# Kernel optimization log

Measured on AMD Instinct MI355X. Metric: run time of the kernel, lower is better.

Reference implementation:

```python
import jax, jax.numpy as jnp
import numpy as np

D_MODEL = 1024
NHEAD = 16
HEAD_DIM = D_MODEL // NHEAD
D_FF = 4096
EPS = 1e-5


def _layernorm(x, g, b):
    mu = jnp.mean(x, axis=-1, keepdims=True)
    var = jnp.mean((x - mu) ** 2, axis=-1, keepdims=True)
    return (x - mu) * jax.lax.rsqrt(var + EPS) * g + b


def setup_inputs() -> dict:
    key = jax.random.key(0)
    ks = jax.random.split(key, 13)
    s = 1.0 / np.sqrt(D_MODEL)
    sf = 1.0 / np.sqrt(D_FF)
    # weights stored as [in, out] (transposed torch Linear)
    return {
        "src": jax.random.normal(ks[0], (4, 2048, D_MODEL), jnp.float32),
        "Wq": jax.random.uniform(ks[1], (D_MODEL, D_MODEL), jnp.float32, -s, s),
        "bq": jnp.zeros((D_MODEL,), jnp.float32),
        "Wk": jax.random.uniform(ks[2], (D_MODEL, D_MODEL), jnp.float32, -s, s),
        "bk": jnp.zeros((D_MODEL,), jnp.float32),
        "Wv": jax.random.uniform(ks[3], (D_MODEL, D_MODEL), jnp.float32, -s, s),
        "bv": jnp.zeros((D_MODEL,), jnp.float32),
        "Wo": jax.random.uniform(ks[4], (D_MODEL, D_MODEL), jnp.float32, -s, s),
        "bo": jnp.zeros((D_MODEL,), jnp.float32),
        "W1": jax.random.uniform(ks[5], (D_MODEL, D_FF), jnp.float32, -s, s),
        "b1": jnp.zeros((D_FF,), jnp.float32),
        "W2": jax.random.uniform(ks[6], (D_FF, D_MODEL), jnp.float32, -sf, sf),
        "b2": jnp.zeros((D_MODEL,), jnp.float32),
        "g1": jnp.ones((D_MODEL,), jnp.float32),
        "be1": jnp.zeros((D_MODEL,), jnp.float32),
        "g2": jnp.ones((D_MODEL,), jnp.float32),
        "be2": jnp.zeros((D_MODEL,), jnp.float32),
    }


def reference(src, Wq, bq, Wk, bk, Wv, bv, Wo, bo, W1, b1, W2, b2, g1, be1, g2, be2):
    B, S, _ = src.shape
    scale = 1.0 / np.sqrt(HEAD_DIM)
    # project and split heads: [B, H, S, Dh]
    def heads(W, b):
        return (src @ W + b).reshape(B, S, NHEAD, HEAD_DIM).transpose(0, 2, 1, 3)
    Q, K, V = heads(Wq, bq), heads(Wk, bk), heads(Wv, bv)
    scores = jnp.einsum('bhqd,bhkd->bhqk', Q, K) * scale
    attn = jax.nn.softmax(scores, axis=-1)
    ctx = jnp.einsum('bhqk,bhkd->bhqd', attn, V)
    ctx = ctx.transpose(0, 2, 1, 3).reshape(B, S, D_MODEL)
    attn_out = ctx @ Wo + bo
    x = _layernorm(src + attn_out, g1, be1)
    ff = jax.nn.relu(x @ W1 + b1) @ W2 + b2
    return _layernorm(x + ff, g2, be2)
```

## Files before the change

### kernel.cpp

```cpp
#include <hip/hip_runtime.h>

typedef __attribute__((ext_vector_type(8))) short bf16x8;
typedef __attribute__((ext_vector_type(4))) float f32x4;
typedef unsigned short u16;
typedef unsigned int u32;

__device__ __forceinline__ u16 f2b(float f) {
  u32 u = __float_as_uint(f);
  u = (u + 0x7fffu + ((u >> 16) & 1u)) >> 16;
  return (u16)u;
}
__device__ __forceinline__ float b2f(u16 b) {
  return __uint_as_float(((u32)b) << 16);
}
__device__ __forceinline__ u32 cvtpk_bf16(float lo, float hi) {
  u32 r;
  asm("v_cvt_pk_bf16_f32 %0, %1, %2" : "=v"(r) : "v"(lo), "v"(hi));
  return r;
}
__device__ __forceinline__ void gload_lds16(const u16* g, u16* l) {
  __builtin_amdgcn_global_load_lds(
      (const __attribute__((address_space(1))) void*)g,
      (__attribute__((address_space(3))) void*)l, 16, 0, 0);
}

__device__ __forceinline__ void tr_tile(const float* __restrict__ in,
                                        u16* __restrict__ out, int R, int C,
                                        int bx, int by, int tid) {
  __shared__ float t[32][33];
  int tx = tid & 31, ty = tid >> 5;
  int rb = by * 32, cb = bx * 32;
  for (int i = 0; i < 4; i++)
    t[ty + i * 8][tx] = in[(size_t)(rb + ty + i * 8) * C + cb + tx];
  __syncthreads();
  for (int i = 0; i < 4; i++)
    out[(size_t)(cb + ty + i * 8) * R + rb + tx] = f2b(t[tx][ty + i * 8]);
}

__global__ __launch_bounds__(256) void prep(
    const float* __restrict__ src, u16* __restrict__ XB,
    const float* __restrict__ Wq, const float* __restrict__ Wk,
    const float* __restrict__ Wv, const float* __restrict__ Wo,
    const float* __restrict__ W1, const float* __restrict__ W2,
    u16* __restrict__ WQKVT, u16* __restrict__ WOT, u16* __restrict__ W1T,
    u16* __restrict__ W2T, const float* __restrict__ bq,
    const float* __restrict__ bk, const float* __restrict__ bv,
    float* __restrict__ bqkv) {
  const int blk = blockIdx.x, tid = threadIdx.x;
  if (blk < 8192) {
    int i = blk * 256 + tid;
    float4 v = ((const float4*)src)[i];
    ushort4 o;
    o.x = f2b(v.x); o.y = f2b(v.y); o.z = f2b(v.z); o.w = f2b(v.w);
    ((ushort4*)XB)[i] = o;
  } else if (blk < 8192 + 4096) {
    int t = blk - 8192;
    int w = t >> 10, tt = t & 1023;
    const float* in = (w == 0) ? Wq : (w == 1) ? Wk : (w == 2) ? Wv : Wo;
    u16* out = (w == 3) ? WOT : (WQKVT + (size_t)w * 1024 * 1024);
    tr_tile(in, out, 1024, 1024, tt & 31, tt >> 5, tid);
  } else if (blk < 8192 + 4096 + 4096) {
    int t = blk - (8192 + 4096);
    tr_tile(W1, W1T, 1024, 4096, t & 127, t >> 7, tid);
  } else if (blk < 8192 + 4096 + 4096 + 4096) {
    int t = blk - (8192 + 4096 + 4096);
    tr_tile(W2, W2T, 4096, 1024, t & 31, t >> 5, tid);
  } else {
    int i = (blk - (8192 + 4096 + 4096 + 4096)) * 256 + tid;
    if (i < 3072)
      bqkv[i] = i < 1024 ? bq[i] : (i < 2048 ? bk[i - 1024] : bv[i - 2048]);
  }
}

__device__ __forceinline__ void stage_quarter(const u16* __restrict__ src,
                                              size_t rowbase, int K, int kcol,
                                              u16* dst, int c, int srow, int sg,
                                              int wid) {
  int row_ = c * 64 + srow;
  int gs_ = sg ^ (row_ & 7);
  gload_lds16(src + (rowbase + row_) * K + kcol + gs_ * 8,
              &dst[(c * 64 + wid * 8) * 64]);
}

template <bool PF>
__device__ __forceinline__ void tile_step(
    const u16* sAc, const u16* sBc, u16* sAn, u16* sBn,
    const u16* __restrict__ A, const u16* __restrict__ Bt, size_t abase,
    size_t bbase, int K, int Tn, int wm, int wn, int l16, int lq, int srow,
    int sg, int wid, f32x4 (&acc)[8][4]) {
  __syncthreads();
#pragma unroll
  for (int ks = 0; ks < 2; ++ks) {
    bf16x8 Bf[4], Af[4];
#pragma unroll
    for (int j = 0; j < 4; ++j) {
      int r = wn * 64 + j * 16 + l16;
      Bf[j] = *(const bf16x8*)&sBc[r * 64 + (((ks * 4 + lq) ^ (r & 7)) << 3)];
    }
#pragma unroll
    for (int i = 0; i < 4; ++i) {
      int r = wm * 128 + i * 16 + l16;
      Af[i] = *(const bf16x8*)&sAc[r * 64 + (((ks * 4 + lq) ^ (r & 7)) << 3)];
    }
    if (PF) {
      const u16* src = (ks == 0) ? A : Bt;
      size_t rb = (ks == 0) ? abase : bbase;
      u16* dst = (ks == 0) ? sAn : sBn;
      stage_quarter(src, rb, K, Tn * 64, dst, 0, srow, sg, wid);
      stage_quarter(src, rb, K, Tn * 64, dst, 1, srow, sg, wid);
    }
    __builtin_amdgcn_s_setprio(1);
#pragma unroll
    for (int i = 0; i < 4; ++i)
#pragma unroll
      for (int j = 0; j < 4; ++j)
        acc[i][j] = __builtin_amdgcn_mfma_f32_16x16x32_bf16(Af[i], Bf[j],
                                                            acc[i][j], 0, 0, 0);
    __builtin_amdgcn_s_setprio(0);
#pragma unroll
    for (int i = 0; i < 4; ++i) {
      int r = wm * 128 + 64 + i * 16 + l16;
      Af[i] = *(const bf16x8*)&sAc[r * 64 + (((ks * 4 + lq) ^ (r & 7)) << 3)];
    }
    if (PF) {
      const u16* src = (ks == 0) ? A : Bt;
      size_t rb = (ks == 0) ? abase : bbase;
      u16* dst = (ks == 0) ? sAn : sBn;
      stage_quarter(src, rb, K, Tn * 64, dst, 2, srow, sg, wid);
      stage_quarter(src, rb, K, Tn * 64, dst, 3, srow, sg, wid);
    }
    __builtin_amdgcn_s_setprio(1);
#pragma unroll
    for (int i = 0; i < 4; ++i)
#pragma unroll
      for (int j = 0; j < 4; ++j)
        acc[4 + i][j] = __builtin_amdgcn_mfma_f32_16x16x32_bf16(
            Af[i], Bf[j], acc[4 + i][j], 0, 0, 0);
    __builtin_amdgcn_s_setprio(0);
  }
}

template <int MODE>
__global__ __launch_bounds__(512, 1) void gemm256(const u16* __restrict__ A,
                                                  const u16* __restrict__ Bt,
                                                  const float* __restrict__ bias,
                                                  void* __restrict__ out,
                                                  int M, int N, int K,
                                                  float oscale) {
  __shared__ u16 sA0[256 * 64];
  __shared__ u16 sB0[256 * 64];
  __shared__ u16 sA1[256 * 64];
  __shared__ u16 sB1[256 * 64];
  const int tid = threadIdx.x, lane = tid & 63, wid = tid >> 6;
  const int l16 = lane & 15, lq = lane >> 4;
  const int wm = wid >> 2, wn = wid & 3;
  const size_t abase = (size_t)blockIdx.x * 256;
  const size_t bbase = (size_t)blockIdx.y * 256;
  const int srow = tid >> 3;
  const int sg = tid & 7;
  const int nt = K >> 6;

  f32x4 acc[8][4];
#pragma unroll
  for (int i = 0; i < 8; ++i)
#pragma unroll
    for (int j = 0; j < 4; ++j) acc[i][j] = (f32x4){0.f, 0.f, 0.f, 0.f};

#pragma unroll
  for (int c = 0; c < 4; ++c) {
    stage_quarter(A, abase, K, 0, sA0, c, srow, sg, wid);
    stage_quarter(Bt, bbase, K, 0, sB0, c, srow, sg, wid);
  }

  int T = 0;
  for (; T + 2 < nt; T += 2) {
    tile_step<true>(sA0, sB0, sA1, sB1, A, Bt, abase, bbase, K, T + 1, wm, wn,
                    l16, lq, srow, sg, wid, acc);
    tile_step<true>(sA1, sB1, sA0, sB0, A, Bt, abase, bbase, K, T + 2, wm, wn,
                    l16, lq, srow, sg, wid, acc);
  }
  tile_step<true>(sA0, sB0, sA1, sB1, A, Bt, abase, bbase, K, nt - 1, wm, wn,
                  l16, lq, srow, sg, wid, acc);
  tile_step<false>(sA1, sB1, sA0, sB0, A, Bt, abase, bbase, K, 0, wm, wn, l16,
                   lq, srow, sg, wid, acc);

  const int gmb = blockIdx.x * 256 + wm * 128;
  const int gnb = blockIdx.y * 256 + wn * 64;
#pragma unroll
  for (int i = 0; i < 8; ++i) {
    int gm0 = gmb + i * 16 + lq * 4;
#pragma unroll
    for (int j = 0; j < 4; ++j) {
      int gn = gnb + j * 16 + l16;
      float bv = bias[gn];
#pragma unroll
      for (int r = 0; r < 4; ++r) {
        float v = acc[i][j][r] + bv;
        ((u16*)out)[(size_t)(gm0 + r) * N + gn] = f2b(v > 0.f ? v : 0.f);
      }
    }
  }
}

template <bool PF>
__device__ __forceinline__ void tile_stepR(
    const u16* sAc, const u16* sBc, u16* sAn, u16* sBn,
    const u16* __restrict__ A, const u16* __restrict__ Bt, size_t abase,
    size_t bbase, int K, int Tn, int wm, int wn, int l16, int lq, int srow,
    int sg, int wid, f32x4 (&acc)[4][4]) {
  __syncthreads();
#pragma unroll
  for (int ks = 0; ks < 2; ++ks) {
    bf16x8 Bf[4], Af[4];
#pragma unroll
    for (int j = 0; j < 4; ++j) {
      int r = wn * 64 + j * 16 + l16;
      Bf[j] = *(const bf16x8*)&sBc[r * 64 + (((ks * 4 + lq) ^ (r & 7)) << 3)];
    }
#pragma unroll
    for (int i = 0; i < 4; ++i) {
      int r = wm * 64 + i * 16 + l16;
      Af[i] = *(const bf16x8*)&sAc[r * 64 + (((ks * 4 + lq) ^ (r & 7)) << 3)];
    }
    if (PF) {
      if (ks == 0) {
        stage_quarter(A, abase, K, Tn * 64, sAn, 0, srow, sg, wid);
        stage_quarter(A, abase, K, Tn * 64, sAn, 1, srow, sg, wid);
        stage_quarter(Bt, bbase, K, Tn * 64, sBn, 0, srow, sg, wid);
      } else {
        stage_quarter(Bt, bbase, K, Tn * 64, sBn, 1, srow, sg, wid);
        stage_quarter(Bt, bbase, K, Tn * 64, sBn, 2, srow, sg, wid);
        stage_quarter(Bt, bbase, K, Tn * 64, sBn, 3, srow, sg, wid);
      }
    }
    __builtin_amdgcn_s_setprio(1);
#pragma unroll
    for (int i = 0; i < 4; ++i)
#pragma unroll
      for (int j = 0; j < 4; ++j)
        acc[i][j] = __builtin_amdgcn_mfma_f32_16x16x32_bf16(Af[i], Bf[j],
                                                            acc[i][j], 0, 0, 0);
    __builtin_amdgcn_s_setprio(0);
  }
}

template <int MODE>
__global__ __launch_bounds__(512, 1) void gemmR(const u16* __restrict__ A,
                                                const u16* __restrict__ Bt,
                                                const float* __restrict__ bias,
                                                void* __restrict__ out,
                                                int M, int N, int K,
                                                float oscale) {
  __shared__ u16 sA0[128 * 64];
  __shared__ u16 sB0[256 * 64];
  __shared__ u16 sA1[128 * 64];
  __shared__ u16 sB1[256 * 64];
  const int tid = threadIdx.x, lane = tid & 63, wid = tid >> 6;
  const int l16 = lane & 15, lq = lane >> 4;
  const int wm = wid >> 2, wn = wid & 3;
  const size_t abase = (size_t)blockIdx.x * 128;
  const size_t bbase = (size_t)blockIdx.y * 256;
  const int srow = tid >> 3;
  const int sg = tid & 7;
  const int nt = K >> 6;

  f32x4 acc[4][4];
#pragma unroll
  for (int i = 0; i < 4; ++i)
#pragma unroll
    for (int j = 0; j < 4; ++j) acc[i][j] = (f32x4){0.f, 0.f, 0.f, 0.f};

#pragma unroll
  for (int c = 0; c < 2; ++c) stage_quarter(A, abase, K, 0, sA0, c, srow, sg, wid);
#pragma unroll
  for (int c = 0; c < 4; ++c) stage_quarter(Bt, bbase, K, 0, sB0, c, srow, sg, wid);

  int T = 0;
  for (; T + 2 < nt; T += 2) {
    tile_stepR<true>(sA0, sB0, sA1, sB1, A, Bt, abase, bbase, K, T + 1, wm, wn,
                     l16, lq, srow, sg, wid, acc);
    tile_stepR<true>(sA1, sB1, sA0, sB0, A, Bt, abase, bbase, K, T + 2, wm, wn,
                     l16, lq, srow, sg, wid, acc);
  }
  tile_stepR<true>(sA0, sB0, sA1, sB1, A, Bt, abase, bbase, K, nt - 1, wm, wn,
                   l16, lq, srow, sg, wid, acc);
  tile_stepR<false>(sA1, sB1, sA0, sB0, A, Bt, abase, bbase, K, 0, wm, wn, l16,
                    lq, srow, sg, wid, acc);

  const int gmb = blockIdx.x * 128 + wm * 64;
  const int gnb = blockIdx.y * 256 + wn * 64;
#pragma unroll
  for (int i = 0; i < 4; ++i) {
    int gm0 = gmb + i * 16 + lq * 4;
#pragma unroll
    for (int j = 0; j < 4; ++j) {
      int gn = gnb + j * 16 + l16;
      float bv = bias[gn];
      if constexpr (MODE == 1) {
#pragma unroll
        for (int r = 0; r < 4; ++r)
          ((u16*)out)[(size_t)(gm0 + r) * N + gn] = f2b(acc[i][j][r] + bv);
      } else {
        int sel = gn >> 10;
        int h = (gn & 1023) >> 6, d = gn & 63;
        int b = gm0 >> 11, s = gm0 & 2047;
        u16* o = (u16*)out + (size_t)sel * (8u << 20);
        if (sel == 2) {
          ushort4 w;
          w.x = f2b(acc[i][j][0] + bv);
          w.y = f2b(acc[i][j][1] + bv);
          w.z = f2b(acc[i][j][2] + bv);
          w.w = f2b(acc[i][j][3] + bv);
          *(ushort4*)(o + ((size_t)((b * 16 + h) * 64 + d)) * 2048 + s) = w;
        } else {
          float sc = (sel == 0) ? oscale : 1.f;
#pragma unroll
          for (int r = 0; r < 4; ++r)
            o[((size_t)(b * 16 + h) * 2048 + s + r) * 64 + d] =
                f2b((acc[i][j][r] + bv) * sc);
        }
      }
    }
  }
}

__global__ __launch_bounds__(512) void attn_fwd(const u16* __restrict__ Q,
                                                const u16* __restrict__ Kb,
                                                const u16* __restrict__ Vt,
                                                u16* __restrict__ ctx) {
  __shared__ u16 sK[64][64];
  __shared__ u16 sV[64][64];
  __shared__ u16 sP[8][16][72];
  const int tid = threadIdx.x, lane = tid & 63, wid = tid >> 6;
  const int l16 = lane & 15, lq = lane >> 4;
  const int bh = blockIdx.y, qt = blockIdx.x;
  const size_t base = (size_t)bh * (2048 * 64);
  const int xk = l16 & 7;

  bf16x8 qf[2];
  {
    int qrow = qt * 128 + wid * 16 + l16;
    qf[0] = *(const bf16x8*)(Q + base + (size_t)qrow * 64 + lq * 8);
    qf[1] = *(const bf16x8*)(Q + base + (size_t)qrow * 64 + 32 + lq * 8);
  }
  f32x4 o[4];
#pragma unroll
  for (int j = 0; j < 4; j++) o[j] = (f32x4){0.f, 0.f, 0.f, 0.f};
  float lrow = 0.f;

  const int srow = tid >> 3;
  const int sg8 = ((tid & 7) ^ (srow & 7)) * 8;
  const int wslot = (tid & 7) * 8;

  const u16* kp = Kb + base + (size_t)srow * 64 + sg8;
  const u16* vp = Vt + base + (size_t)srow * 2048 + sg8;

  uint4 rk = *(const uint4*)kp;
  uint4 rv = *(const uint4*)vp;

  for (int kv0 = 0; kv0 < 2048; kv0 += 64) {
    __syncthreads();
    *(uint4*)&sK[srow][wslot] = rk;
    *(uint4*)&sV[srow][wslot] = rv;
    if (kv0 + 64 < 2048) {
      int kn = kv0 + 64;
      rk = *(const uint4*)(kp + (size_t)kn * 64);
      rv = *(const uint4*)(vp + kn);
    }
    __syncthreads();

    f32x4 sf[4];
#pragma unroll
    for (int j = 0; j < 4; j++) sf[j] = (f32x4){0.f, 0.f, 0.f, 0.f};
    __builtin_amdgcn_s_setprio(1);
#pragma unroll
    for (int ks = 0; ks < 2; ks++)
#pragma unroll
      for (int j = 0; j < 4; j++) {
        bf16x8 kf = *(const bf16x8*)&sK[j * 16 + l16][((ks * 4 + lq) ^ xk) * 8];
        sf[j] = __builtin_amdgcn_mfma_f32_16x16x32_bf16(kf, qf[ks], sf[j], 0, 0, 0);
      }
    __builtin_amdgcn_s_setprio(0);

#pragma unroll
    for (int j = 0; j < 4; j++) {
      float p0 = __builtin_amdgcn_exp2f(sf[j][0]);
      float p1 = __builtin_amdgcn_exp2f(sf[j][1]);
      float p2 = __builtin_amdgcn_exp2f(sf[j][2]);
      float p3 = __builtin_amdgcn_exp2f(sf[j][3]);
      lrow += (p0 + p1) + (p2 + p3);
      uint2 w;
      w.x = cvtpk_bf16(p0, p1);
      w.y = cvtpk_bf16(p2, p3);
      *(uint2*)&sP[wid][l16][j * 16 + lq * 4] = w;
    }

    __builtin_amdgcn_s_setprio(1);
#pragma unroll
    for (int ks = 0; ks < 2; ks++) {
      bf16x8 pf = *(const bf16x8*)&sP[wid][l16][ks * 32 + lq * 8];
#pragma unroll
      for (int j = 0; j < 4; j++) {
        bf16x8 vf = *(const bf16x8*)&sV[j * 16 + l16][((ks * 4 + lq) ^ xk) * 8];
        o[j] = __builtin_amdgcn_mfma_f32_16x16x32_bf16(pf, vf, o[j], 0, 0, 0);
      }
    }
    __builtin_amdgcn_s_setprio(0);
  }

  lrow += __shfl_xor(lrow, 16);
  lrow += __shfl_xor(lrow, 32);
  float lval[4];
#pragma unroll
  for (int r = 0; r < 4; r++) lval[r] = 1.f / __shfl(lrow, lq * 4 + r);
  const int b = bh >> 4, h = bh & 15;
#pragma unroll
  for (int j = 0; j < 4; j++)
#pragma unroll
    for (int r = 0; r < 4; r++) {
      int srw = qt * 128 + wid * 16 + lq * 4 + r;
      int d = j * 16 + l16;
      ctx[((size_t)(b * 2048 + srw)) * 1024 + h * 64 + d] = f2b(o[j][r] * lval[r]);
    }
}

template <int A_BF16, int B_BF16, int WRITE_F32>
__global__ __launch_bounds__(256) void ln_res(const void* __restrict__ a,
                                              const void* __restrict__ bsrc,
                                              const float* __restrict__ g,
                                              const float* __restrict__ be,
                                              float* __restrict__ outf,
                                              u16* __restrict__ outb) {
  const int row = blockIdx.x, tid = threadIdx.x;
  const size_t off = (size_t)row * 1024 + tid * 4;
  float4 x;
  if constexpr (A_BF16) {
    ushort4 av = *(const ushort4*)((const u16*)a + off);
    x.x = b2f(av.x); x.y = b2f(av.y); x.z = b2f(av.z); x.w = b2f(av.w);
  } else {
    x = *(const float4*)((const float*)a + off);
  }
  if constexpr (B_BF16) {
    ushort4 bv = *(const ushort4*)((const u16*)bsrc + off);
    x.x += b2f(bv.x); x.y += b2f(bv.y); x.z += b2f(bv.z); x.w += b2f(bv.w);
  } else {
    float4 bb = *(const float4*)((const float*)bsrc + off);
    x.x += bb.x; x.y += bb.y; x.z += bb.z; x.w += bb.w;
  }
  float s = x.x + x.y + x.z + x.w;
  float s2 = x.x * x.x + x.y * x.y + x.z * x.z + x.w * x.w;
  for (int o = 1; o < 64; o <<= 1) {
    s += __shfl_xor(s, o);
    s2 += __shfl_xor(s2, o);
  }
  __shared__ float rbuf[8];
  int lane = tid & 63, wid = tid >> 6;
  if (lane == 0) { rbuf[wid] = s; rbuf[4 + wid] = s2; }
  __syncthreads();
  s = rbuf[0] + rbuf[1] + rbuf[2] + rbuf[3];
  s2 = rbuf[4] + rbuf[5] + rbuf[6] + rbuf[7];
  float mu = s * (1.f / 1024.f);
  float var = s2 * (1.f / 1024.f) - mu * mu;
  float rstd = rsqrtf(var + 1e-5f);
  int c = tid * 4;
  float y0 = (x.x - mu) * rstd * g[c + 0] + be[c + 0];
  float y1 = (x.y - mu) * rstd * g[c + 1] + be[c + 1];
  float y2 = (x.z - mu) * rstd * g[c + 2] + be[c + 2];
  float y3 = (x.w - mu) * rstd * g[c + 3] + be[c + 3];
  if constexpr (WRITE_F32) {
    float4 y; y.x = y0; y.y = y1; y.z = y2; y.w = y3;
    *(float4*)(outf + off) = y;
  } else {
    ushort4 yb;
    yb.x = f2b(y0); yb.y = f2b(y1); yb.z = f2b(y2); yb.w = f2b(y3);
    *(ushort4*)(outb + off) = yb;
  }
}

extern "C" void kernel_launch(void* const* d_in, const int* in_sizes, int n_in,
                              void* d_out, int out_size, void* d_ws, size_t ws_size,
                              hipStream_t stream) {
  const float* src = (const float*)d_in[0];
  const float* Wq = (const float*)d_in[1];
  const float* bq = (const float*)d_in[2];
  const float* Wk = (const float*)d_in[3];
  const float* bk = (const float*)d_in[4];
  const float* Wv = (const float*)d_in[5];
  const float* bv = (const float*)d_in[6];
  const float* Wo = (const float*)d_in[7];
  const float* bo = (const float*)d_in[8];
  const float* W1 = (const float*)d_in[9];
  const float* b1 = (const float*)d_in[10];
  const float* W2 = (const float*)d_in[11];
  const float* b2 = (const float*)d_in[12];
  const float* g1 = (const float*)d_in[13];
  const float* be1 = (const float*)d_in[14];
  const float* g2 = (const float*)d_in[15];
  const float* be2 = (const float*)d_in[16];
  float* out = (float*)d_out;
  char* ws = (char*)d_ws;
  const size_t MB = 1ull << 20;

  u16* XB    = (u16*)(ws + 0);
  u16* WQKVT = (u16*)(ws + 16 * MB);
  u16* WOT   = (u16*)(ws + 22 * MB);
  u16* W1T   = (u16*)(ws + 24 * MB);
  u16* W2T   = (u16*)(ws + 32 * MB);
  float* bqkv = (float*)(ws + 40 * MB);
  u16* Qb    = (u16*)(ws + 41 * MB);
  u16* Kbuf  = (u16*)(ws + 57 * MB);
  u16* Vt    = (u16*)(ws + 73 * MB);
  u16* CTX   = XB;
  u16* AO    = (u16*)(ws + 41 * MB);
  u16* H1    = (u16*)(ws + 57 * MB);
  u16* XBUF  = (u16*)(ws + 121 * MB);
  u16* FF    = XB;

  const float QSCALE = 0.125f * 1.44269504088896340736f;

  prep<<<dim3(8192 + 4096 + 4096 + 4096 + 13), dim3(256), 0, stream>>>(
      src, XB, Wq, Wk, Wv, Wo, W1, W2, WQKVT, WOT, W1T, W2T, bq, bk, bv, bqkv);

  gemmR<6><<<dim3(64, 12), dim3(512), 0, stream>>>(XB, WQKVT, bqkv, Qb,
                                                   8192, 3072, 1024, QSCALE);
  attn_fwd<<<dim3(16, 64), dim3(512), 0, stream>>>(Qb, Kbuf, Vt, CTX);
  gemmR<1><<<dim3(64, 4), dim3(512), 0, stream>>>(CTX, WOT, bo, AO,
                                                  8192, 1024, 1024, 1.0f);
  ln_res<0, 1, 0><<<dim3(8192), dim3(256), 0, stream>>>(src, AO, g1, be1, nullptr, XBUF);
  gemm256<2><<<dim3(32, 16), dim3(512), 0, stream>>>(XBUF, W1T, b1, H1,
                                                     8192, 4096, 1024, 1.0f);
  gemmR<1><<<dim3(64, 4), dim3(512), 0, stream>>>(H1, W2T, b2, FF,
                                                  8192, 1024, 4096, 1.0f);
  ln_res<1, 1, 1><<<dim3(8192), dim3(256), 0, stream>>>(XBUF, FF, g2, be2, out, nullptr);
}
```

Before: 338.9 us.

## Stage only K in LDS with 128-row tiles and read V fragments from global

The attention kernel now stages 128 K rows per barrier interval in LDS and processes them as two 64-row halves, halving the number of __syncthreads per sequence. V is no longer staged in shared memory. Each wave loads its V^T MFMA fragments directly from global memory, relying on cache reuse across the 8 waves. The aim is to cut LDS traffic and barrier overhead. The cost is redundant global or L2 reads of V with no software prefetch, which may expose memory latency inside the PV MFMA loop.

```diff
diff --git a/kernel.cpp b/kernel.cpp
--- a/kernel.cpp
+++ b/kernel.cpp
@@ -328,8 +328,7 @@
                                                 const u16* __restrict__ Kb,
                                                 const u16* __restrict__ Vt,
                                                 u16* __restrict__ ctx) {
-  __shared__ u16 sK[64][64];
-  __shared__ u16 sV[64][64];
+  __shared__ u16 sK[128][64];
   __shared__ u16 sP[8][16][72];
   const int tid = threadIdx.x, lane = tid & 63, wid = tid >> 6;
   const int l16 = lane & 15, lq = lane >> 4;
@@ -348,64 +347,68 @@
   for (int j = 0; j < 4; j++) o[j] = (f32x4){0.f, 0.f, 0.f, 0.f};
   float lrow = 0.f;
 
-  const int srow = tid >> 3;
-  const int sg8 = ((tid & 7) ^ (srow & 7)) * 8;
-  const int wslot = (tid & 7) * 8;
-
-  const u16* kp = Kb + base + (size_t)srow * 64 + sg8;
-  const u16* vp = Vt + base + (size_t)srow * 2048 + sg8;
-
-  uint4 rk = *(const uint4*)kp;
-  uint4 rv = *(const uint4*)vp;
-
-  for (int kv0 = 0; kv0 < 2048; kv0 += 64) {
+  const int srow = tid >> 2;
+  const int gp = (tid & 3) * 2;
+  const int g0 = gp ^ (srow & 7), g1 = (gp + 1) ^ (srow & 7);
+  const u16* kp0 = Kb + base + (size_t)srow * 64 + g0 * 8;
+  const u16* kp1 = Kb + base + (size_t)srow * 64 + g1 * 8;
+
+  uint4 rk0 = *(const uint4*)kp0;
+  uint4 rk1 = *(const uint4*)kp1;
+
+  for (int kv0 = 0; kv0 < 2048; kv0 += 128) {
     __syncthreads();
-    *(uint4*)&sK[srow][wslot] = rk;
-    *(uint4*)&sV[srow][wslot] = rv;
-    if (kv0 + 64 < 2048) {
-      int kn = kv0 + 64;
-      rk = *(const uint4*)(kp + (size_t)kn * 64);
-      rv = *(const uint4*)(vp + kn);
+    *(uint4*)&sK[srow][gp * 8] = rk0;
+    *(uint4*)&sK[srow][(gp + 1) * 8] = rk1;
+    if (kv0 + 128 < 2048) {
+      int kn = kv0 + 128;
+      rk0 = *(const uint4*)(kp0 + (size_t)kn * 64);
+      rk1 = *(const uint4*)(kp1 + (size_t)kn * 64);
     }
     __syncthreads();
 
-    f32x4 sf[4];
-#pragma unroll
-    for (int j = 0; j < 4; j++) sf[j] = (f32x4){0.f, 0.f, 0.f, 0.f};
-    __builtin_amdgcn_s_setprio(1);
-#pragma unroll
-    for (int ks = 0; ks < 2; ks++)
+#pragma unroll
+    for (int ht = 0; ht < 2; ++ht) {
+      f32x4 sf[4];
+#pragma unroll
+      for (int j = 0; j < 4; j++) sf[j] = (f32x4){0.f, 0.f, 0.f, 0.f};
+      __builtin_amdgcn_s_setprio(1);
+#pragma unroll
+      for (int ks = 0; ks < 2; ks++)
+#pragma unroll
+        for (int j = 0; j < 4; j++) {
+          bf16x8 kf =
+              *(const bf16x8*)&sK[ht * 64 + j * 16 + l16][((ks * 4 + lq) ^ xk) * 8];
+          sf[j] = __builtin_amdgcn_mfma_f32_16x16x32_bf16(kf, qf[ks], sf[j], 0, 0, 0);
+        }
+      __builtin_amdgcn_s_setprio(0);
+
 #pragma unroll
       for (int j = 0; j < 4; j++) {
-        bf16x8 kf = *(const bf16x8*)&sK[j * 16 + l16][((ks * 4 + lq) ^ xk) * 8];
-        sf[j] = __builtin_amdgcn_mfma_f32_16x16x32_bf16(kf, qf[ks], sf[j], 0, 0, 0);
+        float p0 = __builtin_amdgcn_exp2f(sf[j][0]);
+        float p1 = __builtin_amdgcn_exp2f(sf[j][1]);
+        float p2 = __builtin_amdgcn_exp2f(sf[j][2]);
+        float p3 = __builtin_amdgcn_exp2f(sf[j][3]);
+        lrow += (p0 + p1) + (p2 + p3);
+        uint2 w;
+        w.x = cvtpk_bf16(p0, p1);
+        w.y = cvtpk_bf16(p2, p3);
+        *(uint2*)&sP[wid][l16][j * 16 + lq * 4] = w;
       }
-    __builtin_amdgcn_s_setprio(0);
-
-#pragma unroll
-    for (int j = 0; j < 4; j++) {
-      float p0 = __builtin_amdgcn_exp2f(sf[j][0]);
-      float p1 = __builtin_amdgcn_exp2f(sf[j][1]);
-      float p2 = __builtin_amdgcn_exp2f(sf[j][2]);
-      float p3 = __builtin_amdgcn_exp2f(sf[j][3]);
-      lrow += (p0 + p1) + (p2 + p3);
-      uint2 w;
-      w.x = cvtpk_bf16(p0, p1);
-      w.y = cvtpk_bf16(p2, p3);
-      *(uint2*)&sP[wid][l16][j * 16 + lq * 4] = w;
-    }
-
-    __builtin_amdgcn_s_setprio(1);
-#pragma unroll
-    for (int ks = 0; ks < 2; ks++) {
-      bf16x8 pf = *(const bf16x8*)&sP[wid][l16][ks * 32 + lq * 8];
-#pragma unroll
-      for (int j = 0; j < 4; j++) {
-        bf16x8 vf = *(const bf16x8*)&sV[j * 16 + l16][((ks * 4 + lq) ^ xk) * 8];
-        o[j] = __builtin_amdgcn_mfma_f32_16x16x32_bf16(pf, vf, o[j], 0, 0, 0);
+
+      __builtin_amdgcn_s_setprio(1);
+#pragma unroll
+      for (int ks = 0; ks < 2; ks++) {
+        bf16x8 pf = *(const bf16x8*)&sP[wid][l16][ks * 32 + lq * 8];
+#pragma unroll
+        for (int j = 0; j < 4; j++) {
+          bf16x8 vf = *(const bf16x8*)(Vt + base + (size_t)(j * 16 + l16) * 2048 +
+                                       kv0 + ht * 64 + ks * 32 + lq * 8);
+          o[j] = __builtin_amdgcn_mfma_f32_16x16x32_bf16(pf, vf, o[j], 0, 0, 0);
+        }
       }
-    }
-    __builtin_amdgcn_s_setprio(0);
+      __builtin_amdgcn_s_setprio(0);
+    }
   }
 
   lrow += __shfl_xor(lrow, 16);
```

Measured after the change: 486.4 us. 43.5% more time.
